# Performance work log

Measured on AMD Instinct MI355X. Metric: run time of the kernel, lower is better.

Reference implementation:

```python
import jax, jax.numpy as jnp
import numpy as np
from jax import lax

B, E = 32, 8
O, I, K = 192, 192, 3
H, W = 56, 56
PAD = 1  # static 'same' padding for k=3, s=1, d=1


def setup_inputs() -> dict:
    key = jax.random.key(0)
    k1, k2, k3, k4 = jax.random.split(key, 4)
    x = jax.random.normal(k1, (B, I, H, W), dtype=jnp.float32)
    routing_weights = jax.random.uniform(k2, (B, E), dtype=jnp.float32)
    weight = jax.random.normal(k3, (E, O * I * K * K), dtype=jnp.float32) * 0.05
    bias = jax.random.normal(k4, (E, O), dtype=jnp.float32) * 0.05
    return {"x": x, "routing_weights": routing_weights, "weight": weight, "bias": bias}


def _condconv(x, routing_weights, weight, bias):
    # Mix expert weights per sample: [B, E] @ [E, O*I*K*K] -> [B, O, I, K, K]
    w = jnp.matmul(routing_weights, weight).reshape(B, O, I, K, K)
    b = jnp.matmul(routing_weights, bias)  # [B, O]

    def conv_one(xi, wi):
        # xi: [I, H, W], wi: [O, I, K, K] -> [O, H, W]
        out = lax.conv_general_dilated(
            xi[None], wi, window_strides=(1, 1),
            padding=[(PAD, PAD), (PAD, PAD)],
            dimension_numbers=("NCHW", "OIHW", "NCHW"))
        return out[0]

    out = jax.vmap(conv_one)(x, w)  # [B, O, H, W]
    return out + b[:, :, None, None]


def reference(x, routing_weights, weight, bias):
    return _condconv(x, routing_weights, weight, bias)
```

## Files before the change

### kernel.cpp

```cpp
#include <hip/hip_runtime.h>
#include <hip/hip_fp16.h>

using f16x8 = __attribute__((ext_vector_type(8))) _Float16;
using f32x4 = __attribute__((ext_vector_type(4))) float;

#define B_ 32
#define E_ 8
#define O_ 192
#define I_ 192
#define H_ 56
#define W_ 56
#define HW_ 3136
#define IK_ 1728
#define WSZ_ (O_ * IK_)

#define WT_E ((size_t)B_ * 9 * 24 * O_ * 8)
#define XT_E ((size_t)B_ * 6 * HW_ * 32)
#define S_STRIDE 36864
#define ICB_STRIDE 100352

__global__ __launch_bounds__(256) void mix_w(
    const float* __restrict__ r, const float* __restrict__ Wt,
    const float* __restrict__ bias, _Float16* __restrict__ wT,
    float* __restrict__ bmix) {
    int gid = blockIdx.x * 256 + threadIdx.x;
    int b = gid / (O_ * I_);
    int rem = gid - b * (O_ * I_);
    int o = rem / I_;
    int i = rem - o * I_;

    float rb[E_];
#pragma unroll
    for (int e = 0; e < E_; ++e) rb[e] = r[b * E_ + e];

    float acc[9];
#pragma unroll
    for (int s = 0; s < 9; ++s) acc[s] = 0.f;
#pragma unroll
    for (int e = 0; e < E_; ++e) {
        const float* wp = Wt + (size_t)e * WSZ_ + (size_t)rem * 9;
#pragma unroll
        for (int s = 0; s < 9; ++s) acc[s] = fmaf(rb[e], wp[s], acc[s]);
    }
    size_t base =
        (((size_t)(b * 9) * 24 + (i >> 3)) * O_ + o) * 8 + (i & 7);
#pragma unroll
    for (int s = 0; s < 9; ++s)
        wT[base + (size_t)s * S_STRIDE] = (_Float16)acc[s];

    if (i == 0) {
        float bacc = 0.f;
#pragma unroll
        for (int e = 0; e < E_; ++e)
            bacc = fmaf(rb[e], bias[e * O_ + o], bacc);
        bmix[b * O_ + o] = bacc;
    }
}

__global__ __launch_bounds__(256) void xsplit(const float* __restrict__ x,
                                              _Float16* __restrict__ xT) {
    __shared__ float tile[64][65];
    int t = threadIdx.x, tx = t & 63, ty = t >> 6;
    int b = blockIdx.z, i0 = blockIdx.y * 64, hw0 = blockIdx.x * 64;
    const float* xb = x + ((size_t)b * I_ + i0) * HW_ + hw0;
#pragma unroll
    for (int k = 0; k < 16; ++k) {
        int il = ty * 16 + k;
        tile[il][tx] = xb[(size_t)il * HW_ + tx];
    }
    __syncthreads();
    int i = i0 + tx;
#pragma unroll
    for (int k = 0; k < 16; ++k) {
        int hwl = ty * 16 + k;
        xT[(((size_t)b * 6 + (i >> 5)) * HW_ + hw0 + hwl) * 32 + (i & 31)] =
            (_Float16)tile[tx][hwl];
    }
}

__global__ __launch_bounds__(256, 3) void conv_f16(
    const _Float16* __restrict__ xT, const _Float16* __restrict__ wT,
    const float* __restrict__ bmix, float* __restrict__ out) {
    __shared__ __align__(16) unsigned char xs[2][22272];

    const int t = threadIdx.x;
    const int lane = t & 63, wv = t >> 6;
    const int lc = lane & 15, g = lane >> 4;
    const int h0 = blockIdx.x * 4;
    const int ob = blockIdx.y * 96 + (wv >> 1) * 48;
    const int pbase = (wv & 1) * 112;
    const int b = blockIdx.z;

    int rowbase[7];
#pragma unroll
    for (int f = 0; f < 7; ++f) {
        int ploc = pbase + f * 16 + lc;
        rowbase[f] = (ploc / 56) * 58 + (ploc % 56);
    }

    int soff[6];
    int qoff[6];
#pragma unroll
    for (int q = 0; q < 6; ++q) {
        int idx = q * 256 + t;
        if (idx < 1392) {
            int row = idx >> 2, c = idx & 3;
            int rr = row / 58, ww = row - rr * 58;
            soff[q] = row * 64 + (((c ^ (row >> 1)) & 3) << 4);
            int h = h0 - 1 + rr, w = ww - 1;
            if ((unsigned)h < (unsigned)H_ && (unsigned)w < (unsigned)W_)
                qoff[q] = (((b * 6) * HW_ + h * W_ + w) << 5) + c * 8;
            else
                qoff[q] = -1;
        } else {
            soff[q] = -1;
            qoff[q] = -1;
        }
    }

    f16x8 stg[6];
    const f16x8 zero8 = (f16x8){0, 0, 0, 0, 0, 0, 0, 0};

#define LOADSTAGE(icb)                                                      \
    {                                                                       \
        _Pragma("unroll") for (int q = 0; q < 6; ++q) {                     \
            stg[q] = (qoff[q] >= 0)                                         \
                         ? *(const f16x8*)(xT + qoff[q] +                   \
                                           (icb) * ICB_STRIDE)              \
                         : zero8;                                           \
        }                                                                   \
    }
#define WRITESTAGE(buf)                                                     \
    {                                                                       \
        _Pragma("unroll") for (int q = 0; q < 6; ++q) {                     \
            if (soff[q] >= 0) *(f16x8*)(xs[buf] + soff[q]) = stg[q];        \
        }                                                                   \
    }

    f32x4 acc[3][7];
#pragma unroll
    for (int mi = 0; mi < 3; ++mi)
#pragma unroll
        for (int f = 0; f < 7; ++f) acc[mi][f] = (f32x4){0.f, 0.f, 0.f, 0.f};

    LOADSTAGE(0);
    WRITESTAGE(0);
    LOADSTAGE(1);
    __syncthreads();

    for (int k = 0; k < 6; ++k) {
        const int buf = k & 1;
#pragma unroll
        for (int s = 0; s < 9; ++s) {
            const int dh = s / 3, dw = s - dh * 3;
            f16x8 ah[3];
#pragma unroll
            for (int mi = 0; mi < 3; ++mi)
                ah[mi] = *(const f16x8*)(wT +
                                         ((((size_t)(b * 9 + s) * 24 +
                                            k * 4 + g) *
                                               O_ +
                                           (ob + mi * 16 + lc))
                                          << 3));
#pragma unroll
            for (int f = 0; f < 7; ++f) {
                int row = rowbase[f] + dh * 58 + dw;
                int off = row * 64 + (((g ^ (row >> 1)) & 3) << 4);
                f16x8 bv = *(const f16x8*)(xs[buf] + off);
#pragma unroll
                for (int mi = 0; mi < 3; ++mi)
                    acc[mi][f] = __builtin_amdgcn_mfma_f32_16x16x32_f16(
                        ah[mi], bv, acc[mi][f], 0, 0, 0);
            }
        }
        if (k < 5) {
            WRITESTAGE(buf ^ 1);
            if (k < 4) LOADSTAGE(k + 2);
            __syncthreads();
        }
    }

#pragma unroll
    for (int mi = 0; mi < 3; ++mi) {
#pragma unroll
        for (int j = 0; j < 4; ++j) {
            int o = ob + mi * 16 + g * 4 + j;
            float bs = bmix[b * O_ + o];
            float* op = out + ((size_t)(b * O_ + o)) * HW_ + (size_t)h0 * W_;
#pragma unroll
            for (int f = 0; f < 7; ++f) {
                int ploc = pbase + f * 16 + lc;
                op[ploc] = acc[mi][f][j] + bs;
            }
        }
    }
#undef LOADSTAGE
#undef WRITESTAGE
}

__global__ __launch_bounds__(256, 2) void condconv_fp32(
    const float* __restrict__ x, const float* __restrict__ wsrc,
    const float* __restrict__ r, const float* __restrict__ bias,
    float* __restrict__ out) {
    __shared__ float xsf[16][6][58];
    __shared__ float wsm[16 * 9][68];
    const int t = threadIdx.x;
    const int wg = t & 7, hg = (t >> 3) & 1, og = t >> 4;
    const int h0 = blockIdx.x * 4, o0 = blockIdx.y * 64, b = blockIdx.z;
    const float* xb = x + (size_t)b * I_ * H_ * W_;
    float rb[E_];
#pragma unroll
    for (int e = 0; e < E_; ++e) rb[e] = r[b * E_ + e];
    float acc[4][2][7];
#pragma unroll
    for (int oo = 0; oo < 4; ++oo)
#pragma unroll
        for (int hh = 0; hh < 2; ++hh)
#pragma unroll
            for (int ww = 0; ww < 7; ++ww) acc[oo][hh][ww] = 0.f;
    for (int ic = 0; ic < I_; ic += 16) {
        __syncthreads();
        for (int idx = t; idx < 16 * 6 * 58; idx += 256) {
            int ch = idx / (6 * 58), rem = idx - ch * (6 * 58);
            int rr = rem / 58, cc = rem - rr * 58;
            int hgl = h0 - 1 + rr, wgl = cc - 1;
            float v = 0.f;
            if ((unsigned)hgl < H_ && (unsigned)wgl < W_)
                v = xb[(size_t)(ic + ch) * (H_ * W_) + hgl * W_ + wgl];
            ((float*)xsf)[idx] = v;
        }
        for (int idx = t; idx < 64 * 144; idx += 256) {
            int o = idx / 144, ikl = idx - o * 144;
            float v = 0.f;
#pragma unroll
            for (int e = 0; e < E_; ++e)
                v = fmaf(rb[e],
                         wsrc[(size_t)e * WSZ_ + (size_t)(o0 + o) * IK_ +
                              ic * 9 + ikl],
                         v);
            wsm[ikl][o] = v;
        }
        __syncthreads();
        for (int i = 0; i < 16; ++i) {
#pragma unroll
            for (int kh = 0; kh < 3; ++kh) {
                float xr[2][9];
#pragma unroll
                for (int hh = 0; hh < 2; ++hh)
#pragma unroll
                    for (int c = 0; c < 9; ++c)
                        xr[hh][c] = xsf[i][hg * 2 + hh + kh][wg * 7 + c];
#pragma unroll
                for (int kw = 0; kw < 3; ++kw) {
                    float4 wv =
                        *(const float4*)&wsm[i * 9 + kh * 3 + kw][og * 4];
                    float wreg[4] = {wv.x, wv.y, wv.z, wv.w};
#pragma unroll
                    for (int oo = 0; oo < 4; ++oo)
#pragma unroll
                        for (int hh = 0; hh < 2; ++hh)
#pragma unroll
                            for (int ww = 0; ww < 7; ++ww)
                                acc[oo][hh][ww] =
                                    fmaf(wreg[oo], xr[hh][kw + ww],
                                         acc[oo][hh][ww]);
                }
            }
        }
    }
#pragma unroll
    for (int oo = 0; oo < 4; ++oo) {
        int o = o0 + og * 4 + oo;
        float bs = 0.f;
#pragma unroll
        for (int e = 0; e < E_; ++e) bs = fmaf(rb[e], bias[e * O_ + o], bs);
        float* ob = out + ((size_t)b * O_ + o) * (H_ * W_);
#pragma unroll
        for (int hh = 0; hh < 2; ++hh) {
            int h = h0 + hg * 2 + hh;
#pragma unroll
            for (int ww = 0; ww < 7; ++ww)
                ob[h * W_ + wg * 7 + ww] = acc[oo][hh][ww] + bs;
        }
    }
}

extern "C" void kernel_launch(void* const* d_in, const int* in_sizes, int n_in,
                              void* d_out, int out_size, void* d_ws,
                              size_t ws_size, hipStream_t stream) {
    const float* x = (const float*)d_in[0];
    const float* r = (const float*)d_in[1];
    const float* Wt = (const float*)d_in[2];
    const float* bias = (const float*)d_in[3];
    float* out = (float*)d_out;

    const size_t need = WT_E * 2 + XT_E * 2 + (size_t)B_ * O_ * 4;

    if (ws_size >= need) {
        unsigned char* p = (unsigned char*)d_ws;
        _Float16* wT = (_Float16*)p;
        p += WT_E * 2;
        _Float16* xT = (_Float16*)p;
        p += XT_E * 2;
        float* bmix = (float*)p;

        mix_w<<<(B_ * O_ * I_) / 256, 256, 0, stream>>>(r, Wt, bias, wT, bmix);
        xsplit<<<dim3(HW_ / 64, I_ / 64, B_), 256, 0, stream>>>(x, xT);
        conv_f16<<<dim3(H_ / 4, 2, B_), 256, 0, stream>>>(xT, wT, bmix, out);
    } else {
        condconv_fp32<<<dim3(H_ / 4, O_ / 64, B_), 256, 0, stream>>>(x, Wt, r,
                                                                     bias, out);
    }
}
```

Before: 499.0 us.

## Restructure expert-weight mixing and retile conv over all outputs with XCD-aware mapping

mix_w now loads each expert weight slice once per block and loops over the batch, writing 16-byte vectorized f16 outputs, so the expert weight tensor is no longer re-read once per sample. conv_f16 changes its tiling: each block covers 2 output rows and all 192 output channels, with 4 waves splitting the output channels. This replaces the old 4-row by 96-channel blocks and shrinks the LDS input tile. A 1-D grid maps blocks of the same batch onto the same XCD to improve L2 reuse of that sample's weights and inputs. The trade-off is more blocks, and more input-halo reloading per output row.

```diff
diff --git a/kernel.cpp b/kernel.cpp
--- a/kernel.cpp
+++ b/kernel.cpp
@@ -16,44 +16,49 @@
 
 #define WT_E ((size_t)B_ * 9 * 24 * O_ * 8)
 #define XT_E ((size_t)B_ * 6 * HW_ * 32)
-#define S_STRIDE 36864
-#define ICB_STRIDE 100352
-
-__global__ __launch_bounds__(256) void mix_w(
+#define ICB_STRIDE (HW_ * 32)
+
+__global__ __launch_bounds__(192) void mix_w(
     const float* __restrict__ r, const float* __restrict__ Wt,
     const float* __restrict__ bias, _Float16* __restrict__ wT,
     float* __restrict__ bmix) {
-    int gid = blockIdx.x * 256 + threadIdx.x;
-    int b = gid / (O_ * I_);
-    int rem = gid - b * (O_ * I_);
-    int o = rem / I_;
-    int i = rem - o * I_;
-
-    float rb[E_];
-#pragma unroll
-    for (int e = 0; e < E_; ++e) rb[e] = r[b * E_ + e];
-
-    float acc[9];
-#pragma unroll
-    for (int s = 0; s < 9; ++s) acc[s] = 0.f;
-#pragma unroll
-    for (int e = 0; e < E_; ++e) {
-        const float* wp = Wt + (size_t)e * WSZ_ + (size_t)rem * 9;
-#pragma unroll
-        for (int s = 0; s < 9; ++s) acc[s] = fmaf(rb[e], wp[s], acc[s]);
-    }
-    size_t base =
-        (((size_t)(b * 9) * 24 + (i >> 3)) * O_ + o) * 8 + (i & 7);
-#pragma unroll
-    for (int s = 0; s < 9; ++s)
-        wT[base + (size_t)s * S_STRIDE] = (_Float16)acc[s];
-
-    if (i == 0) {
-        float bacc = 0.f;
-#pragma unroll
-        for (int e = 0; e < E_; ++e)
-            bacc = fmaf(rb[e], bias[e * O_ + o], bacc);
-        bmix[b * O_ + o] = bacc;
+    const int t = threadIdx.x;
+    const int s = blockIdx.x % 9;
+    const int i8 = blockIdx.x / 9;
+
+    float we[64];
+#pragma unroll
+    for (int e = 0; e < E_; ++e)
+#pragma unroll
+        for (int j = 0; j < 8; ++j)
+            we[e * 8 + j] =
+                Wt[(size_t)e * WSZ_ + (size_t)t * IK_ + (i8 * 8 + j) * 9 + s];
+
+    for (int b = 0; b < B_; ++b) {
+        float acc[8];
+#pragma unroll
+        for (int j = 0; j < 8; ++j) acc[j] = 0.f;
+#pragma unroll
+        for (int e = 0; e < E_; ++e) {
+            float rv = r[b * E_ + e];
+#pragma unroll
+            for (int j = 0; j < 8; ++j)
+                acc[j] = fmaf(rv, we[e * 8 + j], acc[j]);
+        }
+        f16x8 v;
+#pragma unroll
+        for (int j = 0; j < 8; ++j) v[j] = (_Float16)acc[j];
+        *(f16x8*)(wT + ((((size_t)(b * 9 + s)) * 24 + i8) * O_ + t) * 8) = v;
+    }
+
+    if (blockIdx.x == 0) {
+        for (int b = 0; b < B_; ++b) {
+            float bacc = 0.f;
+#pragma unroll
+            for (int e = 0; e < E_; ++e)
+                bacc = fmaf(r[b * E_ + e], bias[e * O_ + t], bacc);
+            bmix[b * O_ + t] = bacc;
+        }
     }
 }
 
@@ -81,35 +86,39 @@
 __global__ __launch_bounds__(256, 3) void conv_f16(
     const _Float16* __restrict__ xT, const _Float16* __restrict__ wT,
     const float* __restrict__ bmix, float* __restrict__ out) {
-    __shared__ __align__(16) unsigned char xs[2][22272];
+    __shared__ __align__(16) unsigned char xs[2][14848];
 
     const int t = threadIdx.x;
     const int lane = t & 63, wv = t >> 6;
     const int lc = lane & 15, g = lane >> 4;
-    const int h0 = blockIdx.x * 4;
-    const int ob = blockIdx.y * 96 + (wv >> 1) * 48;
-    const int pbase = (wv & 1) * 112;
-    const int b = blockIdx.z;
+
+    const int gsw = blockIdx.x;
+    const int xcd = gsw & 7;
+    const int rest = gsw >> 3;
+    const int hb = rest % 28;
+    const int b = (rest / 28) * 8 + xcd;
+    const int h0 = hb * 2;
+    const int ob = wv * 48;
 
     int rowbase[7];
 #pragma unroll
     for (int f = 0; f < 7; ++f) {
-        int ploc = pbase + f * 16 + lc;
+        int ploc = f * 16 + lc;
         rowbase[f] = (ploc / 56) * 58 + (ploc % 56);
     }
 
-    int soff[6];
-    int qoff[6];
-#pragma unroll
-    for (int q = 0; q < 6; ++q) {
+    int soff[4];
+    int qoff[4];
+#pragma unroll
+    for (int q = 0; q < 4; ++q) {
         int idx = q * 256 + t;
-        if (idx < 1392) {
+        if (idx < 928) {
             int row = idx >> 2, c = idx & 3;
             int rr = row / 58, ww = row - rr * 58;
             soff[q] = row * 64 + (((c ^ (row >> 1)) & 3) << 4);
             int h = h0 - 1 + rr, w = ww - 1;
             if ((unsigned)h < (unsigned)H_ && (unsigned)w < (unsigned)W_)
-                qoff[q] = (((b * 6) * HW_ + h * W_ + w) << 5) + c * 8;
+                qoff[q] = ((b * 6) * HW_ + h * W_ + w) * 32 + c * 8;
             else
                 qoff[q] = -1;
         } else {
@@ -118,23 +127,23 @@
         }
     }
 
-    f16x8 stg[6];
+    f16x8 stg[4];
     const f16x8 zero8 = (f16x8){0, 0, 0, 0, 0, 0, 0, 0};
 
-#define LOADSTAGE(icb)                                                      \
-    {                                                                       \
-        _Pragma("unroll") for (int q = 0; q < 6; ++q) {                     \
-            stg[q] = (qoff[q] >= 0)                                         \
-                         ? *(const f16x8*)(xT + qoff[q] +                   \
-                                           (icb) * ICB_STRIDE)              \
-                         : zero8;                                           \
-        }                                                                   \
-    }
-#define WRITESTAGE(buf)                                                     \
-    {                                                                       \
-        _Pragma("unroll") for (int q = 0; q < 6; ++q) {                     \
-            if (soff[q] >= 0) *(f16x8*)(xs[buf] + soff[q]) = stg[q];        \
-        }                                                                   \
+#define LOADSTAGE(icb)                                                       \
+    {                                                                        \
+        _Pragma("unroll") for (int q = 0; q < 4; ++q) {                      \
+            stg[q] = (qoff[q] >= 0)                                          \
+                         ? *(const f16x8*)(xT + qoff[q] +                    \
+                                           (icb) * ICB_STRIDE)               \
+                         : zero8;                                            \
+        }                                                                    \
+    }
+#define WRITESTAGE(buf)                                                      \
+    {                                                                        \
+        _Pragma("unroll") for (int q = 0; q < 4; ++q) {                      \
+            if (soff[q] >= 0) *(f16x8*)(xs[buf] + soff[q]) = stg[q];         \
+        }                                                                    \
     }
 
     f32x4 acc[3][7];
@@ -157,11 +166,11 @@
 #pragma unroll
             for (int mi = 0; mi < 3; ++mi)
                 ah[mi] = *(const f16x8*)(wT +
-                                         ((((size_t)(b * 9 + s) * 24 +
-                                            k * 4 + g) *
-                                               O_ +
-                                           (ob + mi * 16 + lc))
-                                          << 3));
+                                         ((((size_t)(b * 9 + s)) * 24 +
+                                           k * 4 + g) *
+                                              O_ +
+                                          (ob + mi * 16 + lc)) *
+                                             8);
 #pragma unroll
             for (int f = 0; f < 7; ++f) {
                 int row = rowbase[f] + dh * 58 + dw;
@@ -189,8 +198,8 @@
             float* op = out + ((size_t)(b * O_ + o)) * HW_ + (size_t)h0 * W_;
 #pragma unroll
             for (int f = 0; f < 7; ++f) {
-                int ploc = pbase + f * 16 + lc;
-                op[ploc] = acc[mi][f][j] + bs;
+                int ploc = f * 16 + lc;
+                op[(ploc / 56) * W_ + (ploc % 56)] = acc[mi][f][j] + bs;
             }
         }
     }
@@ -304,9 +313,9 @@
         p += XT_E * 2;
         float* bmix = (float*)p;
 
-        mix_w<<<(B_ * O_ * I_) / 256, 256, 0, stream>>>(r, Wt, bias, wT, bmix);
+        mix_w<<<9 * 24, 192, 0, stream>>>(r, Wt, bias, wT, bmix);
         xsplit<<<dim3(HW_ / 64, I_ / 64, B_), 256, 0, stream>>>(x, xT);
-        conv_f16<<<dim3(H_ / 4, 2, B_), 256, 0, stream>>>(xT, wT, bmix, out);
+        conv_f16<<<dim3(28 * B_), 256, 0, stream>>>(xT, wT, bmix, out);
     } else {
         condconv_fp32<<<dim3(H_ / 4, O_ / 64, B_), 256, 0, stream>>>(x, Wt, r,
                                                                      bias, out);
```

New measurement: 446.7 us. 10.5% less time.
